# Kernel optimization log

Hardware: AMD Instinct MI355X
Metric: run time of the kernel (lower is better)

Reference implementation:

```python
import jax, jax.numpy as jnp
import numpy as np

L = 3
ALPHA = 1.0
BETA = 1.0
SCALING = 3.0
N_NODES = 100000
N_EDGES = 1250000
D_FEAT = 64


def spmm(row, col, w, z, n):
    # out[i] = sum_{e: row_e == i} w_e * z[col_e]  (torch_sparse.matmul reduce='sum')
    return jax.ops.segment_sum(z[col] * w[:, None], row, num_segments=n)


def setup_inputs() -> dict:
    key = jax.random.key(0)
    k1, k2, k3, k4 = jax.random.split(key, 4)
    x = jax.random.normal(k1, (N_NODES, D_FEAT), dtype=jnp.float32)
    edge_index = jax.random.randint(k2, (2, N_EDGES), 0, N_NODES, dtype=jnp.int64)
    # surrogate for symmetric-normalized adjacency weights
    edge_weight = jax.random.uniform(k3, (N_EDGES,), dtype=jnp.float32) * 0.2
    gammas = jnp.full((L + 1, 1), min(1.0 / SCALING, 1.0), dtype=jnp.float32)
    return {"x": x, "edge_index": edge_index, "edge_weight": edge_weight, "gammas": gammas}


def reference(x, edge_index, edge_weight, gammas):
    n = x.shape[0]
    row, col = edge_index[0], edge_index[1]
    a, b = ALPHA, BETA

    zs = [x]  # z_0 = x
    # l = 1: c * z0 + (a+b+2)/2 * A z0
    z1 = ((a - b) / 2) * zs[-1] + ((a + b + 2) / 2) * spmm(row, col, edge_weight, zs[-1], n)
    zs.append(z1)
    for l in range(2, L + 1):
        c0 = 2 * l * (l + a + b) * (2 * l + a + b - 2)
        c1 = (2 * l + a + b - 1) * (a ** 2 - b ** 2)
        c2 = (2 * l + a + b - 1) * (2 * l + a + b) * (2 * l + a + b - 2)
        c3 = 2 * (l + a - 1) * (l + b - 1) * (2 * l + a + b)
        Az = spmm(row, col, edge_weight, zs[-1], n)
        z = (c1 * zs[-1] + c2 * Az - c3 * zs[-2]) / c0
        zs.append(z)

    coefs = jnp.cumprod(jnp.tanh(gammas) * SCALING, axis=0)  # [L+1, 1]
    Z = jnp.stack(zs, axis=1)  # [N, L+1, d]
    return (Z * coefs).mean(axis=1)
```

## Files before the change

### kernel.cpp

```cpp
#include <hip/hip_runtime.h>
#include <hip/hip_fp16.h>
#include <math.h>

#define D 64
#define RB_SHIFT 6
#define RB 64
#define CAP 1024
#define CAPE 2048
#define MAX_NB 1600
#define LDSE 2048


__global__ void bin_scatter_kernel(const int* __restrict__ row, const int* __restrict__ col,
                                   const float* __restrict__ w,
                                   int* __restrict__ cursor,
                                   int2* __restrict__ binned, int E, int NB) {
    __shared__ int lbase[MAX_NB];
    __shared__ int lcur[MAX_NB];
    int chunk = (E + gridDim.x - 1) / gridDim.x;
    int lo = blockIdx.x * chunk;
    int hi = min(E, lo + chunk);
    for (int j = threadIdx.x; j < NB; j += blockDim.x) { lbase[j] = 0; lcur[j] = 0; }
    __syncthreads();
    for (int i = lo + threadIdx.x; i < hi; i += blockDim.x)
        atomicAdd(&lbase[row[i] >> RB_SHIFT], 1);
    __syncthreads();
    for (int j = threadIdx.x; j < NB; j += blockDim.x) {
        int c = lbase[j];
        int base = c ? atomicAdd(&cursor[j], c) : 0;
        lbase[j] = j * CAP + base;
    }
    __syncthreads();
    for (int i = lo + threadIdx.x; i < hi; i += blockDim.x) {
        int r = row[i];
        int b = r >> RB_SHIFT;
        int off = atomicAdd(&lcur[b], 1);
        binned[lbase[b] + off] = make_int2(col[i] | ((r & (RB - 1)) << 17), __float_as_int(w[i]));
    }
}

__global__ void bucket_sort_kernel(const int2* __restrict__ binned,
                                   const int* __restrict__ cursor,
                                   int2* __restrict__ edges, int2* __restrict__ rowinfo,
                                   int N, int NB) {
    __shared__ int2 perm[CAPE];
    __shared__ int hist[RB];
    __shared__ int plr[RB];
    __shared__ int scn[RB];
    __shared__ int pst[RB];
    __shared__ int cur[RB];
    int b = blockIdx.x, t = threadIdx.x;
    int base = b * CAP;
    int cnt = cursor[b];
    if (cnt > CAP) cnt = CAP;

    if (t < RB) hist[t] = 0;
    __syncthreads();
    for (int i = t; i < cnt; i += 256)
        atomicAdd(&hist[(binned[base + i].x >> 17) & (RB - 1)], 1);
    __syncthreads();
    if (t < RB) plr[t] = (hist[t] + 7) & ~7;
    __syncthreads();
    if (t < RB) scn[t] = max(plr[t], plr[t ^ 1]);
    __syncthreads();
    for (int off = 1; off < RB; off <<= 1) {
        int v = (t < RB && t >= off) ? scn[t - off] : 0;
        __syncthreads();
        if (t < RB) scn[t] += v;
        __syncthreads();
    }
    if (t < RB) {
        int pl = max(plr[t], plr[t ^ 1]);
        int ps = scn[t] - pl;
        pst[t] = ps;
        cur[t] = ps;
    }
    __syncthreads();
    for (int i = t; i < cnt; i += 256) {
        int2 e = binned[base + i];
        int rl = (e.x >> 17) & (RB - 1);
        int d = atomicAdd(&cur[rl], 1);
        __half2 wh2 = __half2half2(__float2half(__int_as_float(e.y)));
        perm[d] = make_int2((e.x & 0x1FFFF) << 7, *(int*)&wh2);
    }
    __syncthreads();
    if (t < RB) {
        int h = hist[t];
        int ps = pst[t];
        int pl = max(plr[t], plr[t ^ 1]);
        int dummycol = (h > 0) ? perm[ps].x : 0;
        for (int i = h; i < pl; ++i) perm[ps + i] = make_int2(dummycol, 0);
        int r0 = b * RB + t;
        if (r0 < N) rowinfo[r0] = make_int2(b * CAPE + ps, pl);
    }
    __syncthreads();
    int ptotal = scn[RB - 1];
    if (ptotal > CAPE) ptotal = CAPE;
    for (int i = t; i < ptotal; i += 256) edges[b * CAPE + i] = perm[i];
}

__global__ void tohalf_kernel(const float4* __restrict__ in, ushort4* __restrict__ o, int n4) {
    int i = blockIdx.x * blockDim.x + threadIdx.x;
    int stride = gridDim.x * blockDim.x;
    for (; i < n4; i += stride) {
        float4 f = in[i];
        ushort4 h;
        h.x = __half_as_ushort(__float2half(f.x));
        h.y = __half_as_ushort(__float2half(f.y));
        h.z = __half_as_ushort(__float2half(f.z));
        h.w = __half_as_ushort(__float2half(f.w));
        o[i] = h;
    }
}

__device__ __forceinline__ __half2 half_row_acc_lds(const int2* __restrict__ lds_desc, int cnt,
                                                    const char* __restrict__ g2b, int koff) {
    __half2 acc = __half2half2(__ushort_as_half((unsigned short)0));
    for (int jb = 0; jb < cnt; jb += 8) {
        int4 dq[4];
        const int4* p4 = (const int4*)(lds_desc + jb);
#pragma unroll
        for (int q = 0; q < 4; ++q) dq[q] = p4[q];
        __half2 v[8];
#pragma unroll
        for (int q = 0; q < 4; ++q) {
            v[2 * q]     = *(const __half2*)(g2b + (size_t)(unsigned)(dq[q].x + koff));
            v[2 * q + 1] = *(const __half2*)(g2b + (size_t)(unsigned)(dq[q].z + koff));
        }
#pragma unroll
        for (int q = 0; q < 4; ++q) {
            acc = __hfma2(*(__half2*)&dq[q].y, v[2 * q], acc);
            acc = __hfma2(*(__half2*)&dq[q].w, v[2 * q + 1], acc);
        }
    }
    return acc;
}

__global__ void spmm_z_kernel(const int2* __restrict__ rowinfo,
                              const int2* __restrict__ edges,
                              const __half2* __restrict__ gsrc2,
                              const __half2* __restrict__ zp2_2,
                              __half2* __restrict__ zdst2,
                              float cA, float cC, int N) {
    __shared__ int2 lds[LDSE];
    int t = threadIdx.x;
    int bid = blockIdx.x;
    int r0 = bid * 8;

    int gs = rowinfo[r0].x;
    int2 rlast = rowinfo[min(r0 + 7, N - 1)];
    int span = rlast.x + rlast.y - gs;
    if (span > LDSE) span = LDSE;
    for (int i = t; i < span; i += 256) lds[i] = edges[gs + i];
    __syncthreads();

    int gid = bid * 256 + t;
    int wv = gid >> 6;
    int lane = t & 63;
    int half = lane >> 5;
    int k = lane & 31;
    int r = 2 * wv + half;
    if (2 * wv >= N) return;
    if (r >= N) r = N - 1;

    int2 ri = rowinfo[r];
    int cnt = __builtin_amdgcn_readfirstlane(ri.y);

    size_t idx2 = (size_t)r * 32 + k;
    float2 p2 = make_float2(0.f, 0.f);
    if (zp2_2) p2 = __half22float2(zp2_2[idx2]);

    __half2 acc = half_row_acc_lds(lds + (ri.x - gs), cnt, (const char*)gsrc2, k * 4);
    float2 a = __half22float2(acc);

    float2 z = make_float2(cA * a.x, cA * a.y);
    if (zp2_2) {
        z.x = fmaf(cC, p2.x, z.x);
        z.y = fmaf(cC, p2.y, z.y);
    }
    zdst2[idx2] = __floats2half2_rn(z.x, z.y);
}

__global__ void spmm_final_kernel(const int2* __restrict__ rowinfo,
                                  const int2* __restrict__ edges,
                                  const __half2* __restrict__ z2h2,
                                  const __half2* __restrict__ z1h2,
                                  const __half2* __restrict__ xh2,
                                  float* __restrict__ out,
                                  const float* __restrict__ gammas,
                                  float cA, float cC, int N) {
    __shared__ int2 lds[LDSE];
    int t = threadIdx.x;
    int bid = blockIdx.x;
    int r0 = bid * 8;

    int gs = rowinfo[r0].x;
    int2 rlast = rowinfo[min(r0 + 7, N - 1)];
    int span = rlast.x + rlast.y - gs;
    if (span > LDSE) span = LDSE;
    for (int i = t; i < span; i += 256) lds[i] = edges[gs + i];
    __syncthreads();

    int gid = bid * 256 + t;
    int wv = gid >> 6;
    int lane = t & 63;
    int half = lane >> 5;
    int k = lane & 31;
    int r = 2 * wv + half;
    if (2 * wv >= N) return;
    if (r >= N) r = N - 1;

    float t0 = tanhf(gammas[0]) * 3.0f;
    float t1 = t0 * (tanhf(gammas[1]) * 3.0f);
    float t2 = t1 * (tanhf(gammas[2]) * 3.0f);
    float t3 = t2 * (tanhf(gammas[3]) * 3.0f);

    int2 ri = rowinfo[r];
    int cnt = __builtin_amdgcn_readfirstlane(ri.y);

    size_t idx2 = (size_t)r * 32 + k;
    float2 z1v = __half22float2(z1h2[idx2]);
    float2 z2v = __half22float2(z2h2[idx2]);
    float2 xv  = __half22float2(xh2[idx2]);

    __half2 acc = half_row_acc_lds(lds + (ri.x - gs), cnt, (const char*)z2h2, k * 4);
    float2 a = __half22float2(acc);

    float2 z3 = make_float2(cA * a.x + cC * z1v.x, cA * a.y + cC * z1v.y);
    float2 o;
    o.x = 0.25f * (t0 * xv.x + t1 * z1v.x + t2 * z2v.x + t3 * z3.x);
    o.y = 0.25f * (t0 * xv.y + t1 * z1v.y + t2 * z2v.y + t3 * z3.y);
    ((float2*)out)[idx2] = o;
}

extern "C" void kernel_launch(void* const* d_in, const int* in_sizes, int n_in,
                              void* d_out, int out_size, void* d_ws, size_t ws_size,
                              hipStream_t stream) {
    const float* x      = (const float*)d_in[0];
    const int*   ei     = (const int*)d_in[1];
    const float* w      = (const float*)d_in[2];
    const float* gammas = (const float*)d_in[3];

    const int E = in_sizes[1] / 2;
    const int N = in_sizes[0] / D;
    const long NF = (long)N * D;
    const int NB = (N + RB - 1) >> RB_SHIFT;

    float* out = (float*)d_out;

    char* p = (char*)d_ws;
    __half* xh  = (__half*)p;       p += NF * sizeof(__half);
    __half* z1h = (__half*)p;       p += NF * sizeof(__half);
    __half* z2h = (__half*)p;       p += NF * sizeof(__half);
    int* cursor = (int*)p;          p += NB * sizeof(int);
    p = (char*)(((uintptr_t)p + 15) & ~(uintptr_t)15);
    int2* rowinfo = (int2*)p;       p += (size_t)N * sizeof(int2);
    int2* binned = (int2*)p;        p += (size_t)NB * CAP * sizeof(int2);
    int2* edges = (int2*)p;

    const int* row = ei;
    const int* col = ei + E;

    const double a = 1.0, b = 1.0;
    const int blk = 256;

    hipMemsetAsync(cursor, 0, (size_t)NB * sizeof(int), stream);
    bin_scatter_kernel<<<256, 1024, 0, stream>>>(row, col, w, cursor, binned, E, NB);
    bucket_sort_kernel<<<NB, 256, 0, stream>>>(binned, cursor, edges, rowinfo, N, NB);
    tohalf_kernel<<<1024, blk, 0, stream>>>((const float4*)x, (ushort4*)xh, (int)(NF / 4));

    const int nwaves = (N + 1) / 2;
    const int sgrid = (nwaves + 3) / 4;

    {
        float cA = (float)((a + b + 2.0) / 2.0);
        spmm_z_kernel<<<sgrid, blk, 0, stream>>>(rowinfo, edges, (const __half2*)xh,
                                                 nullptr, (__half2*)z1h, cA, 0.0f, N);
    }

    {
        int l = 2;
        double c0 = 2.0 * l * (l + a + b) * (2.0 * l + a + b - 2.0);
        double c2 = (2.0 * l + a + b - 1.0) * (2.0 * l + a + b) * (2.0 * l + a + b - 2.0);
        double c3 = 2.0 * (l + a - 1.0) * (l + b - 1.0) * (2.0 * l + a + b);
        spmm_z_kernel<<<sgrid, blk, 0, stream>>>(rowinfo, edges, (const __half2*)z1h,
                                                 (const __half2*)xh, (__half2*)z2h,
                                                 (float)(c2 / c0), (float)(-c3 / c0), N);
    }

    {
        int l = 3;
        double c0 = 2.0 * l * (l + a + b) * (2.0 * l + a + b - 2.0);
        double c2 = (2.0 * l + a + b - 1.0) * (2.0 * l + a + b) * (2.0 * l + a + b - 2.0);
        double c3 = 2.0 * (l + a - 1.0) * (l + b - 1.0) * (2.0 * l + a + b);
        spmm_final_kernel<<<sgrid, blk, 0, stream>>>(rowinfo, edges, (const __half2*)z2h,
                                                     (const __half2*)z1h, (const __half2*)xh,
                                                     out, gammas,
                                                     (float)(c2 / c0), (float)(-c3 / c0), N);
    }
}
```

Baseline: 201.0 us.

## Process four rows per wave with 8-byte gathers in SpMM kernels

The SpMM kernels now map 16 lanes to one row, so each wave covers four rows instead of two. Each lane gathers 8 bytes (four halves) per edge into two accumulators, which halves the number of gather instructions per edge. To keep the 4-edge loop step valid for rows that share a wave, the bucket sort now pads each row to a multiple of 4 and to the max length within a quad of rows. LDS staging and edge copy-out use 16-byte vector accesses, and blocks now cover 16 rows. The change trades wider per-lane loads and less padding for quad-level load imbalance between rows.

```diff
diff --git a/kernel.cpp b/kernel.cpp
--- a/kernel.cpp
+++ b/kernel.cpp
@@ -43,7 +43,7 @@
                                    const int* __restrict__ cursor,
                                    int2* __restrict__ edges, int2* __restrict__ rowinfo,
                                    int N, int NB) {
-    __shared__ int2 perm[CAPE];
+    __shared__ alignas(16) int2 perm[CAPE];
     __shared__ int hist[RB];
     __shared__ int plr[RB];
     __shared__ int scn[RB];
@@ -59,9 +59,12 @@
     for (int i = t; i < cnt; i += 256)
         atomicAdd(&hist[(binned[base + i].x >> 17) & (RB - 1)], 1);
     __syncthreads();
-    if (t < RB) plr[t] = (hist[t] + 7) & ~7;
-    __syncthreads();
-    if (t < RB) scn[t] = max(plr[t], plr[t ^ 1]);
+    if (t < RB) plr[t] = (hist[t] + 3) & ~3;
+    __syncthreads();
+    if (t < RB) {
+        int qb = t & ~3;
+        scn[t] = max(max(plr[qb], plr[qb | 1]), max(plr[qb | 2], plr[qb | 3]));
+    }
     __syncthreads();
     for (int off = 1; off < RB; off <<= 1) {
         int v = (t < RB && t >= off) ? scn[t - off] : 0;
@@ -70,7 +73,8 @@
         __syncthreads();
     }
     if (t < RB) {
-        int pl = max(plr[t], plr[t ^ 1]);
+        int qb = t & ~3;
+        int pl = max(max(plr[qb], plr[qb | 1]), max(plr[qb | 2], plr[qb | 3]));
         int ps = scn[t] - pl;
         pst[t] = ps;
         cur[t] = ps;
@@ -87,7 +91,8 @@
     if (t < RB) {
         int h = hist[t];
         int ps = pst[t];
-        int pl = max(plr[t], plr[t ^ 1]);
+        int qb = t & ~3;
+        int pl = max(max(plr[qb], plr[qb | 1]), max(plr[qb | 2], plr[qb | 3]));
         int dummycol = (h > 0) ? perm[ps].x : 0;
         for (int i = h; i < pl; ++i) perm[ps + i] = make_int2(dummycol, 0);
         int r0 = b * RB + t;
@@ -96,7 +101,10 @@
     __syncthreads();
     int ptotal = scn[RB - 1];
     if (ptotal > CAPE) ptotal = CAPE;
-    for (int i = t; i < ptotal; i += 256) edges[b * CAPE + i] = perm[i];
+    int n4 = ptotal >> 1;
+    const int4* ps4 = (const int4*)perm;
+    int4* pd4 = (int4*)(edges + (size_t)b * CAPE);
+    for (int i = t; i < n4; i += 256) pd4[i] = ps4[i];
 }
 
 __global__ void tohalf_kernel(const float4* __restrict__ in, ushort4* __restrict__ o, int n4) {
@@ -113,27 +121,28 @@
     }
 }
 
-__device__ __forceinline__ __half2 half_row_acc_lds(const int2* __restrict__ lds_desc, int cnt,
-                                                    const char* __restrict__ g2b, int koff) {
-    __half2 acc = __half2half2(__ushort_as_half((unsigned short)0));
-    for (int jb = 0; jb < cnt; jb += 8) {
-        int4 dq[4];
+__device__ __forceinline__ void quad_row_acc_lds(const int2* __restrict__ lds_desc, int cnt,
+                                                 const char* __restrict__ g2b, int boff,
+                                                 __half2& acc0, __half2& acc1) {
+    acc0 = __half2half2(__ushort_as_half((unsigned short)0));
+    acc1 = acc0;
+    for (int jb = 0; jb < cnt; jb += 4) {
         const int4* p4 = (const int4*)(lds_desc + jb);
-#pragma unroll
-        for (int q = 0; q < 4; ++q) dq[q] = p4[q];
-        __half2 v[8];
-#pragma unroll
-        for (int q = 0; q < 4; ++q) {
-            v[2 * q]     = *(const __half2*)(g2b + (size_t)(unsigned)(dq[q].x + koff));
-            v[2 * q + 1] = *(const __half2*)(g2b + (size_t)(unsigned)(dq[q].z + koff));
-        }
-#pragma unroll
-        for (int q = 0; q < 4; ++q) {
-            acc = __hfma2(*(__half2*)&dq[q].y, v[2 * q], acc);
-            acc = __hfma2(*(__half2*)&dq[q].w, v[2 * q + 1], acc);
-        }
-    }
-    return acc;
+        int4 d0 = p4[0];
+        int4 d1 = p4[1];
+        int2 g0 = *(const int2*)(g2b + (size_t)(unsigned)(d0.x + boff));
+        int2 g1 = *(const int2*)(g2b + (size_t)(unsigned)(d0.z + boff));
+        int2 g2 = *(const int2*)(g2b + (size_t)(unsigned)(d1.x + boff));
+        int2 g3 = *(const int2*)(g2b + (size_t)(unsigned)(d1.z + boff));
+        acc0 = __hfma2(*(__half2*)&d0.y, *(__half2*)&g0.x, acc0);
+        acc1 = __hfma2(*(__half2*)&d0.y, *(__half2*)&g0.y, acc1);
+        acc0 = __hfma2(*(__half2*)&d0.w, *(__half2*)&g1.x, acc0);
+        acc1 = __hfma2(*(__half2*)&d0.w, *(__half2*)&g1.y, acc1);
+        acc0 = __hfma2(*(__half2*)&d1.y, *(__half2*)&g2.x, acc0);
+        acc1 = __hfma2(*(__half2*)&d1.y, *(__half2*)&g2.y, acc1);
+        acc0 = __hfma2(*(__half2*)&d1.w, *(__half2*)&g3.x, acc0);
+        acc1 = __hfma2(*(__half2*)&d1.w, *(__half2*)&g3.y, acc1);
+    }
 }
 
 __global__ void spmm_z_kernel(const int2* __restrict__ rowinfo,
@@ -142,43 +151,64 @@
                               const __half2* __restrict__ zp2_2,
                               __half2* __restrict__ zdst2,
                               float cA, float cC, int N) {
-    __shared__ int2 lds[LDSE];
+    __shared__ alignas(16) int2 lds[LDSE];
     int t = threadIdx.x;
     int bid = blockIdx.x;
-    int r0 = bid * 8;
+    int r0 = bid * 16;
 
     int gs = rowinfo[r0].x;
-    int2 rlast = rowinfo[min(r0 + 7, N - 1)];
+    int2 rlast = rowinfo[min(r0 + 15, N - 1)];
     int span = rlast.x + rlast.y - gs;
     if (span > LDSE) span = LDSE;
-    for (int i = t; i < span; i += 256) lds[i] = edges[gs + i];
-    __syncthreads();
-
-    int gid = bid * 256 + t;
-    int wv = gid >> 6;
+    {
+        int n4 = span >> 1;
+        const int4* s4 = (const int4*)(edges + gs);
+        int4* d4 = (int4*)lds;
+        for (int i = t; i < n4; i += 256) d4[i] = s4[i];
+    }
+    __syncthreads();
+
+    int wv = t >> 6;
     int lane = t & 63;
-    int half = lane >> 5;
-    int k = lane & 31;
-    int r = 2 * wv + half;
-    if (2 * wv >= N) return;
-    if (r >= N) r = N - 1;
+    int q = lane >> 4;
+    int k16 = lane & 15;
+    int rr = r0 + wv * 4 + q;
+    bool valid = rr < N;
+    int r = valid ? rr : N - 1;
 
     int2 ri = rowinfo[r];
     int cnt = __builtin_amdgcn_readfirstlane(ri.y);
-
-    size_t idx2 = (size_t)r * 32 + k;
-    float2 p2 = make_float2(0.f, 0.f);
-    if (zp2_2) p2 = __half22float2(zp2_2[idx2]);
-
-    __half2 acc = half_row_acc_lds(lds + (ri.x - gs), cnt, (const char*)gsrc2, k * 4);
-    float2 a = __half22float2(acc);
-
-    float2 z = make_float2(cA * a.x, cA * a.y);
+    int off = ri.x - gs;
+    if (off < 0 || off + cnt > span) off = 0;
+
+    int boff = k16 * 8;
+    size_t rb = (size_t)r * 128 + boff;
+    float2 p0 = make_float2(0.f, 0.f), p1 = p0;
     if (zp2_2) {
-        z.x = fmaf(cC, p2.x, z.x);
-        z.y = fmaf(cC, p2.y, z.y);
-    }
-    zdst2[idx2] = __floats2half2_rn(z.x, z.y);
+        int2 pz = *(const int2*)((const char*)zp2_2 + rb);
+        p0 = __half22float2(*(__half2*)&pz.x);
+        p1 = __half22float2(*(__half2*)&pz.y);
+    }
+
+    __half2 acc0, acc1;
+    quad_row_acc_lds(lds + off, cnt, (const char*)gsrc2, boff, acc0, acc1);
+    float2 a0 = __half22float2(acc0);
+    float2 a1 = __half22float2(acc1);
+
+    float2 z0 = make_float2(cA * a0.x, cA * a0.y);
+    float2 z1 = make_float2(cA * a1.x, cA * a1.y);
+    if (zp2_2) {
+        z0.x = fmaf(cC, p0.x, z0.x); z0.y = fmaf(cC, p0.y, z0.y);
+        z1.x = fmaf(cC, p1.x, z1.x); z1.y = fmaf(cC, p1.y, z1.y);
+    }
+    if (valid) {
+        __half2 h0 = __floats2half2_rn(z0.x, z0.y);
+        __half2 h1 = __floats2half2_rn(z1.x, z1.y);
+        int2 st;
+        st.x = *(int*)&h0;
+        st.y = *(int*)&h1;
+        *(int2*)((char*)zdst2 + rb) = st;
+    }
 }
 
 __global__ void spmm_final_kernel(const int2* __restrict__ rowinfo,
@@ -189,26 +219,30 @@
                                   float* __restrict__ out,
                                   const float* __restrict__ gammas,
                                   float cA, float cC, int N) {
-    __shared__ int2 lds[LDSE];
+    __shared__ alignas(16) int2 lds[LDSE];
     int t = threadIdx.x;
     int bid = blockIdx.x;
-    int r0 = bid * 8;
+    int r0 = bid * 16;
 
     int gs = rowinfo[r0].x;
-    int2 rlast = rowinfo[min(r0 + 7, N - 1)];
+    int2 rlast = rowinfo[min(r0 + 15, N - 1)];
     int span = rlast.x + rlast.y - gs;
     if (span > LDSE) span = LDSE;
-    for (int i = t; i < span; i += 256) lds[i] = edges[gs + i];
-    __syncthreads();
-
-    int gid = bid * 256 + t;
-    int wv = gid >> 6;
+    {
+        int n4 = span >> 1;
+        const int4* s4 = (const int4*)(edges + gs);
+        int4* d4 = (int4*)lds;
+        for (int i = t; i < n4; i += 256) d4[i] = s4[i];
+    }
+    __syncthreads();
+
+    int wv = t >> 6;
     int lane = t & 63;
-    int half = lane >> 5;
-    int k = lane & 31;
-    int r = 2 * wv + half;
-    if (2 * wv >= N) return;
-    if (r >= N) r = N - 1;
+    int q = lane >> 4;
+    int k16 = lane & 15;
+    int rr = r0 + wv * 4 + q;
+    bool valid = rr < N;
+    int r = valid ? rr : N - 1;
 
     float t0 = tanhf(gammas[0]) * 3.0f;
     float t1 = t0 * (tanhf(gammas[1]) * 3.0f);
@@ -217,20 +251,38 @@
 
     int2 ri = rowinfo[r];
     int cnt = __builtin_amdgcn_readfirstlane(ri.y);
-
-    size_t idx2 = (size_t)r * 32 + k;
-    float2 z1v = __half22float2(z1h2[idx2]);
-    float2 z2v = __half22float2(z2h2[idx2]);
-    float2 xv  = __half22float2(xh2[idx2]);
-
-    __half2 acc = half_row_acc_lds(lds + (ri.x - gs), cnt, (const char*)z2h2, k * 4);
-    float2 a = __half22float2(acc);
-
-    float2 z3 = make_float2(cA * a.x + cC * z1v.x, cA * a.y + cC * z1v.y);
-    float2 o;
-    o.x = 0.25f * (t0 * xv.x + t1 * z1v.x + t2 * z2v.x + t3 * z3.x);
-    o.y = 0.25f * (t0 * xv.y + t1 * z1v.y + t2 * z2v.y + t3 * z3.y);
-    ((float2*)out)[idx2] = o;
+    int off = ri.x - gs;
+    if (off < 0 || off + cnt > span) off = 0;
+
+    int boff = k16 * 8;
+    size_t rb = (size_t)r * 128 + boff;
+    int2 pz1 = *(const int2*)((const char*)z1h2 + rb);
+    int2 pz2 = *(const int2*)((const char*)z2h2 + rb);
+    int2 pxv = *(const int2*)((const char*)xh2 + rb);
+
+    __half2 acc0, acc1;
+    quad_row_acc_lds(lds + off, cnt, (const char*)z2h2, boff, acc0, acc1);
+    float2 a0 = __half22float2(acc0);
+    float2 a1 = __half22float2(acc1);
+
+    float2 z1v0 = __half22float2(*(__half2*)&pz1.x);
+    float2 z1v1 = __half22float2(*(__half2*)&pz1.y);
+    float2 z2v0 = __half22float2(*(__half2*)&pz2.x);
+    float2 z2v1 = __half22float2(*(__half2*)&pz2.y);
+    float2 xv0  = __half22float2(*(__half2*)&pxv.x);
+    float2 xv1  = __half22float2(*(__half2*)&pxv.y);
+
+    float2 z30 = make_float2(cA * a0.x + cC * z1v0.x, cA * a0.y + cC * z1v0.y);
+    float2 z31 = make_float2(cA * a1.x + cC * z1v1.x, cA * a1.y + cC * z1v1.y);
+
+    if (valid) {
+        float4 o;
+        o.x = 0.25f * (t0 * xv0.x + t1 * z1v0.x + t2 * z2v0.x + t3 * z30.x);
+        o.y = 0.25f * (t0 * xv0.y + t1 * z1v0.y + t2 * z2v0.y + t3 * z30.y);
+        o.z = 0.25f * (t0 * xv1.x + t1 * z1v1.x + t2 * z2v1.x + t3 * z31.x);
+        o.w = 0.25f * (t0 * xv1.y + t1 * z1v1.y + t2 * z2v1.y + t3 * z31.y);
+        ((float4*)out)[(size_t)r * 16 + k16] = o;
+    }
 }
 
 extern "C" void kernel_launch(void* const* d_in, const int* in_sizes, int n_in,
@@ -269,8 +321,7 @@
     bucket_sort_kernel<<<NB, 256, 0, stream>>>(binned, cursor, edges, rowinfo, N, NB);
     tohalf_kernel<<<1024, blk, 0, stream>>>((const float4*)x, (ushort4*)xh, (int)(NF / 4));
 
-    const int nwaves = (N + 1) / 2;
-    const int sgrid = (nwaves + 3) / 4;
+    const int sgrid = (N + 15) / 16;
 
     {
         float cA = (float)((a + b + 2.0) / 2.0);
```

Measured after the change: 199.5 us. No clear change (-0.7%).
